# Optimization experiments

Measured on AMD Instinct MI355X. Metric: run time of the kernel, lower is better.

The kernel has to match this reference:

```python
import jax, jax.numpy as jnp
import numpy as np

N_NODES = 100000
N_EDGES = 1600000
NEG_SLOPE = 0.2  # PyG GATConv default


def _glorot(key, shape):
    fan = sum(shape[:2]) if len(shape) > 1 else shape[0] * 2
    s = jnp.sqrt(6.0 / fan)
    return jax.random.uniform(key, shape, jnp.float32, -s, s)


def gat_layer(x, src, dst, edge_attr, W, a_src, a_dst, We, a_e, b, heads, out_ch, concat):
    """Faithful PyG GATConv (add_self_loops=True, fill_value='mean', edge_dim set)."""
    n = x.shape[0]
    # self-loop edge_attr = mean of incoming edge_attr per dst node (0 if none)
    deg = jax.ops.segment_sum(jnp.ones((src.shape[0],), edge_attr.dtype), dst, num_segments=n)
    loop_attr = jax.ops.segment_sum(edge_attr, dst, num_segments=n) / jnp.maximum(deg, 1.0)[:, None]
    loop = jnp.arange(n, dtype=src.dtype)
    src_f = jnp.concatenate([src, loop])
    dst_f = jnp.concatenate([dst, loop])
    ea = jnp.concatenate([edge_attr, loop_attr], axis=0)
    # node transform -> [n, H, C]
    h = (x @ W).reshape(n, heads, out_ch)
    al_src = jnp.sum(h * a_src, axis=-1)  # [n, H]
    al_dst = jnp.sum(h * a_dst, axis=-1)  # [n, H]
    e = (ea @ We).reshape(-1, heads, out_ch)
    al_e = jnp.sum(e * a_e, axis=-1)      # [Ef, H]
    alpha = jax.nn.leaky_relu(al_src[src_f] + al_dst[dst_f] + al_e, negative_slope=NEG_SLOPE)
    # segment softmax over destination nodes (every node has a self loop)
    m = jax.ops.segment_max(alpha, dst_f, num_segments=n)
    ex = jnp.exp(alpha - m[dst_f])
    den = jax.ops.segment_sum(ex, dst_f, num_segments=n)
    att = ex / den[dst_f]                 # [Ef, H]
    out = jax.ops.segment_sum(att[:, :, None] * h[src_f], dst_f, num_segments=n)  # [n, H, C]
    out = out.reshape(n, heads * out_ch) if concat else out.mean(axis=1)
    return out + b


def setup_inputs() -> dict:
    key = jax.random.key(0)
    ks = jax.random.split(key, 20)
    x = jax.random.normal(ks[0], (N_NODES, 5), jnp.float32)
    edge_index = jax.random.randint(ks[1], (2, N_EDGES), 0, N_NODES, jnp.int64)
    edge_attr = jax.random.normal(ks[2], (N_EDGES, 2), jnp.float32)
    # conv1: in=5, out=32, heads=4, concat -> 128
    p = {
        "W1": _glorot(ks[3], (5, 128)), "aS1": _glorot(ks[4], (4, 32)),
        "aD1": _glorot(ks[5], (4, 32)), "We1": _glorot(ks[6], (2, 128)),
        "aE1": _glorot(ks[7], (4, 32)), "b1": jnp.zeros((128,), jnp.float32),
        # conv2: in=128, out=32, heads=2, concat -> 64
        "W2": _glorot(ks[8], (128, 64)), "aS2": _glorot(ks[9], (2, 32)),
        "aD2": _glorot(ks[10], (2, 32)), "We2": _glorot(ks[11], (2, 64)),
        "aE2": _glorot(ks[12], (2, 32)), "b2": jnp.zeros((64,), jnp.float32),
        # conv3: in=64, out=1, heads=1, concat=False
        "W3": _glorot(ks[13], (64, 1)), "aS3": _glorot(ks[14], (1, 1)),
        "aD3": _glorot(ks[15], (1, 1)), "We3": _glorot(ks[16], (2, 1)),
        "aE3": _glorot(ks[17], (1, 1)), "b3": jnp.zeros((1,), jnp.float32),
    }
    return {"x": x, "edge_index": edge_index, "edge_attr": edge_attr, **p}


def reference(x, edge_index, edge_attr,
              W1, aS1, aD1, We1, aE1, b1,
              W2, aS2, aD2, We2, aE2, b2,
              W3, aS3, aD3, We3, aE3, b3):
    src, dst = edge_index[0], edge_index[1]
    h = gat_layer(x, src, dst, edge_attr, W1, aS1, aD1, We1, aE1, b1, 4, 32, True)
    h = jax.nn.elu(h)  # dropout is identity in eval
    h = gat_layer(h, src, dst, edge_attr, W2, aS2, aD2, We2, aE2, b2, 2, 32, True)
    h = jax.nn.elu(h)
    h = gat_layer(h, src, dst, edge_attr, W3, aS3, aD3, We3, aE3, b3, 1, 1, False)
    return jax.nn.sigmoid(h).squeeze(-1)  # [N]
```

## Files before the change

### kernel.cpp

```cpp
#include <hip/hip_runtime.h>
#include <math.h>

#define NN 100000
#define NE 1600000
#define NPB 256
#define NB 391
#define NCHUNK 256
#define CH ((NE + NCHUNK - 1) / NCHUNK)
#define LOG2E 1.44269504088896f

__device__ __forceinline__ float lrelu(float x) { return fmaxf(x, 0.2f * x); }
__device__ __forceinline__ float elu1(float x) { return x > 0.f ? x : (__expf(x) - 1.f); }
__device__ __forceinline__ float fexp2(float x) {
#if __has_builtin(__builtin_amdgcn_exp2f)
    return __builtin_amdgcn_exp2f(x);
#else
    return exp2f(x);
#endif
}
__device__ __forceinline__ unsigned bf16rne(float f) {
    unsigned u = __float_as_uint(f);
    return (u + 0x7FFFu + ((u >> 16) & 1u)) >> 16;
}
__device__ __forceinline__ float bf16lo(unsigned u) { return __uint_as_float(u << 16); }
__device__ __forceinline__ float bf16hi(unsigned u) {
    return __uint_as_float(u & 0xFFFF0000u);
}

__global__ void __launch_bounds__(256) k_binA0(const int* __restrict__ dst,
                                               int* __restrict__ bucket_cnt) {
    __shared__ int hist[NB];
    int t = threadIdx.x;
    for (int b = t; b < NB; b += 256) hist[b] = 0;
    __syncthreads();
    int c0 = blockIdx.x * CH, c1 = min(NE, c0 + CH);
    for (int e = c0 + t; e < c1; e += 256) atomicAdd(&hist[dst[e] >> 8], 1);
    __syncthreads();
    for (int b = t; b < NB; b += 256)
        if (hist[b]) atomicAdd(&bucket_cnt[b], hist[b]);
}

__global__ void k_bscan(const int* __restrict__ bucket_cnt, int* __restrict__ bucket_base,
                        int* __restrict__ bucket_tail) {
    __shared__ int s[512];
    int t = threadIdx.x;
    int v = (t < NB) ? bucket_cnt[t] : 0;
    s[t] = v;
    __syncthreads();
    for (int off = 1; off < 512; off <<= 1) {
        int x = (t >= off) ? s[t - off] : 0;
        __syncthreads();
        if (t >= off) s[t] += x;
        __syncthreads();
    }
    if (t < NB) {
        int ex = s[t] - v;
        bucket_base[t] = ex;
        bucket_tail[t] = ex;
        if (t == NB - 1) bucket_base[NB] = s[t];
    }
}

__global__ void __launch_bounds__(256) k_binA2(const int* __restrict__ src,
                                               const int* __restrict__ dst,
                                               const float* __restrict__ ea,
                                               int* __restrict__ bucket_tail,
                                               uint2* __restrict__ binned,
                                               unsigned char* __restrict__ dstb) {
    __shared__ int hist[NB], base_l[NB], cursor[NB];
    int t = threadIdx.x;
    for (int b = t; b < NB; b += 256) {
        hist[b] = 0;
        cursor[b] = 0;
    }
    __syncthreads();
    int c0 = blockIdx.x * CH, c1 = min(NE, c0 + CH);
    for (int e = c0 + t; e < c1; e += 256) atomicAdd(&hist[dst[e] >> 8], 1);
    __syncthreads();
    for (int b = t; b < NB; b += 256)
        if (hist[b]) base_l[b] = atomicAdd(&bucket_tail[b], hist[b]);
    __syncthreads();
    for (int e = c0 + t; e < c1; e += 256) {
        int d = dst[e];
        int bkt = d >> 8;
        int idx = atomicAdd(&cursor[bkt], 1);
        int pos = base_l[bkt] + idx;
        unsigned pk = bf16rne(ea[2 * e]) | (bf16rne(ea[2 * e + 1]) << 16);
        binned[pos] = make_uint2((unsigned)src[e], pk);
        dstb[pos] = (unsigned char)(d & 255);
    }
}

__global__ void __launch_bounds__(256) k_binB(const int* __restrict__ bucket_base,
                                              const uint2* __restrict__ binned,
                                              const unsigned char* __restrict__ dstb,
                                              int* __restrict__ rowptr,
                                              uint2* __restrict__ edges,
                                              float* __restrict__ la) {
    __shared__ int hist[NPB], pre[NPB], cursor[NPB];
    __shared__ float ea0s[NPB], ea1s[NPB];
    int b = blockIdx.x, t = threadIdx.x;
    int bb = bucket_base[b], be = bucket_base[b + 1];
    int nb0 = b << 8;
    hist[t] = 0;
    ea0s[t] = 0.f;
    ea1s[t] = 0.f;
    __syncthreads();
    for (int e = bb + t; e < be; e += 256) atomicAdd(&hist[dstb[e]], 1);
    __syncthreads();
    int v = hist[t];
    pre[t] = v;
    __syncthreads();
    for (int off = 1; off < 256; off <<= 1) {
        int x = (t >= off) ? pre[t - off] : 0;
        __syncthreads();
        if (t >= off) pre[t] += x;
        __syncthreads();
    }
    int ex = pre[t] - v;
    if (nb0 + t <= NN) rowptr[nb0 + t] = bb + ex;
    cursor[t] = bb + ex;
    __syncthreads();
    for (int e = bb + t; e < be; e += 256) {
        uint2 rec = binned[e];
        unsigned char d = dstb[e];
        int pos = atomicAdd(&cursor[d], 1);
        edges[pos] = rec;
        atomicAdd(&ea0s[d], bf16lo(rec.y));
        atomicAdd(&ea1s[d], bf16hi(rec.y));
    }
    __syncthreads();
    int n = nb0 + t;
    if (n < NN) {
        float dg = fmaxf((float)v, 1.0f);
        la[2 * n] = ea0s[t] / dg;
        la[2 * n + 1] = ea1s[t] / dg;
    }
}

__global__ void k_const(const float* __restrict__ We1, const float* __restrict__ aE1,
                        const float* __restrict__ We2, const float* __restrict__ aE2,
                        const float* __restrict__ We3, const float* __restrict__ aE3,
                        const float* __restrict__ W1, const float* __restrict__ aS1,
                        const float* __restrict__ aD1, float* __restrict__ cbuf) {
    int t = threadIdx.x;
    if (t < 8) {
        int d = t >> 2, hd = t & 3;
        float s = 0.f;
        for (int c = 0; c < 32; c++) s += We1[d * 128 + hd * 32 + c] * aE1[hd * 32 + c];
        cbuf[t] = s * LOG2E;
    } else if (t < 12) {
        int idx = t - 8, d = idx >> 1, hd = idx & 1;
        float s = 0.f;
        for (int c = 0; c < 32; c++) s += We2[d * 64 + hd * 32 + c] * aE2[hd * 32 + c];
        cbuf[t] = s * LOG2E;
    } else if (t < 14) {
        cbuf[t] = We3[t - 12] * aE3[0] * LOG2E;
    } else if (t >= 16 && t < 56) {
        int r = (t - 16) % 20, hd = r / 5, i = r % 5;
        const float* a = (t - 16 < 20) ? aS1 : aD1;
        float s = 0.f;
        for (int c = 0; c < 32; c++) s += W1[i * 128 + hd * 32 + c] * a[hd * 32 + c];
        cbuf[t] = s * LOG2E;
    }
}

__global__ void k_prep1(const float* __restrict__ x, const float* __restrict__ vsd,
                        float4* __restrict__ xp, float4* __restrict__ als1,
                        float4* __restrict__ ald1) {
    int n = blockIdx.x * blockDim.x + threadIdx.x;
    if (n >= NN) return;
    float x0 = x[5 * n], x1 = x[5 * n + 1], x2 = x[5 * n + 2], x3 = x[5 * n + 3],
          x4 = x[5 * n + 4];
    xp[2 * n] = make_float4(x0, x1, x2, x3);
    xp[2 * n + 1] = make_float4(x4, 0.f, 0.f, 0.f);
    float sv[4], dv[4];
#pragma unroll
    for (int hd = 0; hd < 4; hd++) {
        const float* vS = vsd + hd * 5;
        const float* vD = vsd + 20 + hd * 5;
        sv[hd] = x0 * vS[0] + x1 * vS[1] + x2 * vS[2] + x3 * vS[3] + x4 * vS[4];
        dv[hd] = x0 * vD[0] + x1 * vD[1] + x2 * vD[2] + x3 * vD[3] + x4 * vD[4];
    }
    als1[n] = make_float4(sv[0], sv[1], sv[2], sv[3]);
    ald1[n] = make_float4(dv[0], dv[1], dv[2], dv[3]);
}

__global__ void k_agg1(const int* __restrict__ rowptr, const uint2* __restrict__ edges,
                       const float4* __restrict__ xp, const float* __restrict__ als1,
                       const float* __restrict__ ald1, const float* __restrict__ la,
                       const float* __restrict__ me, float* __restrict__ xw) {
    int t = blockIdx.x * blockDim.x + threadIdx.x;
    if (t >= NN * 4) return;
    int n = t >> 2, hd = t & 3;
    float me0 = me[hd], me1 = me[4 + hd];
    float aldn = ald1[t];
    float aself = lrelu(als1[t] + aldn + la[2 * n] * me0 + la[2 * n + 1] * me1);
    int start = rowptr[n], end = rowptr[n + 1];
    float den = 1.f;
    float4 xa = xp[2 * n];
    float xb = xp[2 * n + 1].x;
    float a0 = xa.x, a1 = xa.y, a2 = xa.z, a3 = xa.w, a4 = xb;
    for (int e = start; e < end; ++e) {
        uint2 ep = edges[e];
        int s = (int)ep.x;
        float a = lrelu(als1[s * 4 + hd] + aldn + bf16lo(ep.y) * me0 + bf16hi(ep.y) * me1);
        float p = fexp2(a - aself);
        den += p;
        float4 sa = xp[2 * s];
        float sb = xp[2 * s + 1].x;
        a0 += p * sa.x;
        a1 += p * sa.y;
        a2 += p * sa.z;
        a3 += p * sa.w;
        a4 += p * sb;
    }
    float r = 1.f / den;
    float* w = xw + (size_t)n * 20 + hd * 5;
    w[0] = a0 * r;
    w[1] = a1 * r;
    w[2] = a2 * r;
    w[3] = a3 * r;
    w[4] = a4 * r;
}

__global__ void __launch_bounds__(64) k_l2trans(
        const float* __restrict__ xw, const float* __restrict__ W1,
        const float* __restrict__ b1, const float* __restrict__ W2,
        const float* __restrict__ aS2, const float* __restrict__ aD2,
        unsigned short* __restrict__ h2q, float* __restrict__ als2,
        float* __restrict__ ald2) {
    __shared__ float sx[16 * 132];
    int nb = blockIdx.x * 16, t = threadIdx.x;
    {
        int nl = t >> 2, q = t & 3;
        int node = nb + nl;
        float w[20];
        if (node < NN) {
#pragma unroll
            for (int i = 0; i < 20; i++) w[i] = xw[(size_t)node * 20 + i];
        } else {
#pragma unroll
            for (int i = 0; i < 20; i++) w[i] = 0.f;
        }
#pragma unroll
        for (int k = 0; k < 32; k++) {
            int ch = q + 4 * k;
            int hd = ch >> 5;
            float v = w[hd * 5] * W1[ch] + w[hd * 5 + 1] * W1[128 + ch] +
                      w[hd * 5 + 2] * W1[256 + ch] + w[hd * 5 + 3] * W1[384 + ch] +
                      w[hd * 5 + 4] * W1[512 + ch] + b1[ch];
            sx[nl * 132 + ch] = (node < NN) ? elu1(v) : 0.f;
        }
    }
    __syncthreads();
    int jq = t & 15, ng = t >> 4;
    int j4 = jq * 4;
    float4 acc[4];
#pragma unroll
    for (int p = 0; p < 4; p++) acc[p] = make_float4(0.f, 0.f, 0.f, 0.f);
    for (int ic = 0; ic < 128; ic += 4) {
        float4 s[4];
#pragma unroll
        for (int p = 0; p < 4; p++)
            s[p] = *(const float4*)(sx + (ng * 4 + p) * 132 + ic);
#pragma unroll
        for (int r = 0; r < 4; r++) {
            float4 wv = *(const float4*)(W2 + (ic + r) * 64 + j4);
#pragma unroll
            for (int p = 0; p < 4; p++) {
                float sv = (r == 0) ? s[p].x : (r == 1) ? s[p].y : (r == 2) ? s[p].z : s[p].w;
                acc[p].x += sv * wv.x;
                acc[p].y += sv * wv.y;
                acc[p].z += sv * wv.z;
                acc[p].w += sv * wv.w;
            }
        }
    }
    int hd = jq >> 3;
    float4 a_s = *(const float4*)(aS2 + j4);
    float4 a_d = *(const float4*)(aD2 + j4);
    float pS[4], pD[4];
#pragma unroll
    for (int p = 0; p < 4; p++) {
        pS[p] = acc[p].x * a_s.x + acc[p].y * a_s.y + acc[p].z * a_s.z + acc[p].w * a_s.w;
        pD[p] = acc[p].x * a_d.x + acc[p].y * a_d.y + acc[p].z * a_d.z + acc[p].w * a_d.w;
    }
#pragma unroll
    for (int off = 1; off < 8; off <<= 1) {
#pragma unroll
        for (int p = 0; p < 4; p++) {
            pS[p] += __shfl_xor(pS[p], off);
            pD[p] += __shfl_xor(pD[p], off);
        }
    }
#pragma unroll
    for (int p = 0; p < 4; p++) {
        int node = nb + ng * 4 + p;
        if (node < NN) {
            ushort4 q;
            q.x = (unsigned short)bf16rne(acc[p].x);
            q.y = (unsigned short)bf16rne(acc[p].y);
            q.z = (unsigned short)bf16rne(acc[p].z);
            q.w = (unsigned short)bf16rne(acc[p].w);
            *(ushort4*)(h2q + (size_t)node * 64 + j4) = q;
            if ((jq & 7) == 0) {
                als2[node * 2 + hd] = pS[p] * LOG2E;
                ald2[node * 2 + hd] = pD[p] * LOG2E;
            }
        }
    }
}

__global__ void k_agg2(const int* __restrict__ rowptr, const uint2* __restrict__ edges,
                       const unsigned short* __restrict__ h2q,
                       const float* __restrict__ als2, const float* __restrict__ ald2,
                       const float* __restrict__ la, const float* __restrict__ me,
                       const float* __restrict__ b2, const float* __restrict__ W3,
                       float* __restrict__ h3) {
    int t = blockIdx.x * blockDim.x + threadIdx.x;
    if (t >= NN * 4) return;
    int n = t >> 2, sub = t & 3, hd = sub >> 1, qh = sub & 1;
    int cbase = hd * 32 + qh * 16;
    float me0 = me[hd], me1 = me[2 + hd];
    float aldn = ald2[n * 2 + hd];
    float aself = lrelu(als2[n * 2 + hd] + aldn + la[2 * n] * me0 + la[2 * n + 1] * me1);
    int start = rowptr[n], end = rowptr[n + 1];
    float den = 1.f;
    float acc[16];
    {
        const uint4* hp = (const uint4*)(h2q + (size_t)n * 64 + cbase);
        uint4 u0 = hp[0], u1 = hp[1];
        acc[0] = bf16lo(u0.x); acc[1] = bf16hi(u0.x);
        acc[2] = bf16lo(u0.y); acc[3] = bf16hi(u0.y);
        acc[4] = bf16lo(u0.z); acc[5] = bf16hi(u0.z);
        acc[6] = bf16lo(u0.w); acc[7] = bf16hi(u0.w);
        acc[8] = bf16lo(u1.x); acc[9] = bf16hi(u1.x);
        acc[10] = bf16lo(u1.y); acc[11] = bf16hi(u1.y);
        acc[12] = bf16lo(u1.z); acc[13] = bf16hi(u1.z);
        acc[14] = bf16lo(u1.w); acc[15] = bf16hi(u1.w);
    }
    for (int e = start; e < end; ++e) {
        uint2 ep = edges[e];
        int s = (int)ep.x;
        float a = lrelu(als2[s * 2 + hd] + aldn + bf16lo(ep.y) * me0 + bf16hi(ep.y) * me1);
        float p = fexp2(a - aself);
        den += p;
        const uint4* sp = (const uint4*)(h2q + (size_t)s * 64 + cbase);
        uint4 u0 = sp[0], u1 = sp[1];
        acc[0] += p * bf16lo(u0.x); acc[1] += p * bf16hi(u0.x);
        acc[2] += p * bf16lo(u0.y); acc[3] += p * bf16hi(u0.y);
        acc[4] += p * bf16lo(u0.z); acc[5] += p * bf16hi(u0.z);
        acc[6] += p * bf16lo(u0.w); acc[7] += p * bf16hi(u0.w);
        acc[8] += p * bf16lo(u1.x); acc[9] += p * bf16hi(u1.x);
        acc[10] += p * bf16lo(u1.y); acc[11] += p * bf16hi(u1.y);
        acc[12] += p * bf16lo(u1.z); acc[13] += p * bf16hi(u1.z);
        acc[14] += p * bf16lo(u1.w); acc[15] += p * bf16hi(u1.w);
    }
    float r = 1.f / den;
    float part = 0.f;
#pragma unroll
    for (int c = 0; c < 16; c++) {
        float v = elu1(acc[c] * r + b2[cbase + c]);
        part += v * W3[cbase + c];
    }
    part += __shfl_xor(part, 1);
    part += __shfl_xor(part, 2);
    if (sub == 0) h3[n] = part;
}

__global__ void k_agg3(const int* __restrict__ rowptr, const uint2* __restrict__ edges,
                       const float* __restrict__ h, const float* __restrict__ aS3,
                       const float* __restrict__ aD3, const float* __restrict__ la,
                       const float* __restrict__ me, const float* __restrict__ b,
                       float* __restrict__ out) {
    int n = (blockIdx.x * blockDim.x + threadIdx.x) >> 6;
    if (n >= NN) return;
    int lane = threadIdx.x & 63;
    float me0 = me[0], me1 = me[1];
    float aSs = aS3[0] * LOG2E, aDs = aD3[0] * LOG2E;
    float hn = h[n];
    float ald_n = hn * aDs;
    float aself = lrelu(hn * aSs + ald_n + la[2 * n] * me0 + la[2 * n + 1] * me1);
    int start = rowptr[n], end = rowptr[n + 1];
    float den = 0.f, num = 0.f;
    for (int e = start + lane; e < end; e += 64) {
        uint2 ep = edges[e];
        int s = (int)ep.x;
        float hv = h[s];
        float a = lrelu(hv * aSs + ald_n + bf16lo(ep.y) * me0 + bf16hi(ep.y) * me1);
        float p = fexp2(a - aself);
        den += p;
        num += p * hv;
    }
#pragma unroll
    for (int off = 32; off > 0; off >>= 1) {
        den += __shfl_xor(den, off);
        num += __shfl_xor(num, off);
    }
    if (lane == 0) {
        den += 1.f;
        num += hn;
        float v = num / den + b[0];
        out[n] = 1.f / (1.f + __expf(-v));
    }
}

extern "C" void kernel_launch(void* const* d_in, const int* in_sizes, int n_in,
                              void* d_out, int out_size, void* d_ws, size_t ws_size,
                              hipStream_t stream) {
    const float* x   = (const float*)d_in[0];
    const int*   ei  = (const int*)d_in[1];
    const float* ea  = (const float*)d_in[2];
    const float* W1  = (const float*)d_in[3];
    const float* aS1 = (const float*)d_in[4];
    const float* aD1 = (const float*)d_in[5];
    const float* We1 = (const float*)d_in[6];
    const float* aE1 = (const float*)d_in[7];
    const float* b1  = (const float*)d_in[8];
    const float* W2  = (const float*)d_in[9];
    const float* aS2 = (const float*)d_in[10];
    const float* aD2 = (const float*)d_in[11];
    const float* We2 = (const float*)d_in[12];
    const float* aE2 = (const float*)d_in[13];
    const float* b2  = (const float*)d_in[14];
    const float* W3  = (const float*)d_in[15];
    const float* aS3 = (const float*)d_in[16];
    const float* aD3 = (const float*)d_in[17];
    const float* We3 = (const float*)d_in[18];
    const float* aE3 = (const float*)d_in[19];
    const float* b3  = (const float*)d_in[20];

    const int* srcv = ei;
    const int* dstv = ei + NE;

    char* basep = (char*)d_ws;
    size_t off = 0;
    auto alloc = [&](size_t nbytes) -> void* {
        void* p = basep + off;
        off += (nbytes + 255) & ~(size_t)255;
        return p;
    };
    int*    bucket_cnt  = (int*)alloc((size_t)(NB + 1) * 4);
    int*    bucket_base = (int*)alloc((size_t)(NB + 1) * 4);
    int*    bucket_tail = (int*)alloc((size_t)(NB + 1) * 4);
    int*    rowptr      = (int*)alloc((size_t)(NN + 1) * 4);
    uint2*  binned      = (uint2*)alloc((size_t)NE * 8);
    unsigned char* dstb = (unsigned char*)alloc((size_t)NE);
    uint2*  edges       = (uint2*)alloc((size_t)NE * 8);
    float*  la          = (float*)alloc((size_t)NN * 8);
    float*  cbuf        = (float*)alloc(256);
    float4* xp          = (float4*)alloc((size_t)NN * 32);
    float4* als1        = (float4*)alloc((size_t)NN * 16);
    float4* ald1        = (float4*)alloc((size_t)NN * 16);
    float*  xw          = (float*)alloc((size_t)NN * 80);
    unsigned short* h2q = (unsigned short*)alloc((size_t)NN * 128);
    float*  als2        = (float*)alloc((size_t)NN * 8);
    float*  ald2        = (float*)alloc((size_t)NN * 8);
    float*  h3          = (float*)alloc((size_t)NN * 4);
    (void)ws_size; (void)in_sizes; (void)n_in; (void)out_size;

    float* me1 = cbuf;
    float* me2 = cbuf + 8;
    float* me3 = cbuf + 12;
    float* vsd = cbuf + 16;

    auto cdiv = [](long long a, long long b) { return (int)((a + b - 1) / b); };
    const int BS = 256;

    hipMemsetAsync(bucket_cnt, 0, (size_t)(NB + 1) * 4, stream);
    k_binA0<<<NCHUNK, 256, 0, stream>>>(dstv, bucket_cnt);
    k_bscan<<<1, 512, 0, stream>>>(bucket_cnt, bucket_base, bucket_tail);
    k_binA2<<<NCHUNK, 256, 0, stream>>>(srcv, dstv, ea, bucket_tail, binned, dstb);
    k_binB<<<NB, 256, 0, stream>>>(bucket_base, binned, dstb, rowptr, edges, la);

    k_const<<<1, 64, 0, stream>>>(We1, aE1, We2, aE2, We3, aE3, W1, aS1, aD1, cbuf);

    k_prep1<<<cdiv(NN, BS), BS, 0, stream>>>(x, vsd, xp, als1, ald1);
    k_agg1<<<cdiv((long long)NN * 4, BS), BS, 0, stream>>>(rowptr, edges, xp,
                                                           (const float*)als1,
                                                           (const float*)ald1, la, me1, xw);

    k_l2trans<<<cdiv(NN, 16), 64, 0, stream>>>(xw, W1, b1, W2, aS2, aD2, h2q, als2, ald2);
    k_agg2<<<cdiv((long long)NN * 4, BS), BS, 0, stream>>>(rowptr, edges, h2q, als2, ald2,
                                                           la, me2, b2, W3, h3);

    k_agg3<<<cdiv(NN, 4), 256, 0, stream>>>(rowptr, edges, h3, aS3, aD3, la, me3,
                                            b3, (float*)d_out);
}
```

Measured before the change: 344.8 us.

## Fuse edge binning into one local-sort pass and widen layer-2 transform tile

Replaces the separate count pass and scatter pass of edge binning with a single kernel per chunk. Each chunk counts its edges, sorts them locally by bucket in shared memory, writes them out contiguously and records per-chunk segment offsets. The second kernel then gathers each bucket's pieces from all chunks into a shared staging buffer before doing the per-node sort. This is meant to cut one full read of dst and the scattered global writes. Separately, the layer-2 transform now handles 32 nodes per block instead of 16, so each W2 load is reused across more nodes. The fixed MAXB staging cap silently drops edges if a bucket exceeds 5376, so correctness depends on the degree distribution.

```diff
diff --git a/kernel.cpp b/kernel.cpp
--- a/kernel.cpp
+++ b/kernel.cpp
@@ -5,8 +5,10 @@
 #define NE 1600000
 #define NPB 256
 #define NB 391
-#define NCHUNK 256
-#define CH ((NE + NCHUNK - 1) / NCHUNK)
+#define NCHUNK 512
+#define CH 3125
+#define SEGW (NB + 1)
+#define MAXB 5376
 #define LOG2E 1.44269504088896f
 
 __device__ __forceinline__ float lrelu(float x) { return fmaxf(x, 0.2f * x); }
@@ -27,21 +29,59 @@
     return __uint_as_float(u & 0xFFFF0000u);
 }
 
-__global__ void __launch_bounds__(256) k_binA0(const int* __restrict__ dst,
-                                               int* __restrict__ bucket_cnt) {
-    __shared__ int hist[NB];
-    int t = threadIdx.x;
+__global__ void __launch_bounds__(256) k_bin1(const int* __restrict__ src,
+                                              const int* __restrict__ dst,
+                                              const float* __restrict__ ea,
+                                              int* __restrict__ bucket_cnt,
+                                              int* __restrict__ seg,
+                                              uint2* __restrict__ binned,
+                                              unsigned char* __restrict__ dstb) {
+    __shared__ int hist[NB], start[NB], cur[NB];
+    __shared__ int s2[256];
+    __shared__ uint2 stage[CH];
+    __shared__ unsigned char dstg[CH];
+    int c = blockIdx.x, t = threadIdx.x;
+    int e0 = c * CH;
     for (int b = t; b < NB; b += 256) hist[b] = 0;
     __syncthreads();
-    int c0 = blockIdx.x * CH, c1 = min(NE, c0 + CH);
-    for (int e = c0 + t; e < c1; e += 256) atomicAdd(&hist[dst[e] >> 8], 1);
-    __syncthreads();
-    for (int b = t; b < NB; b += 256)
+    for (int i = t; i < CH; i += 256) atomicAdd(&hist[dst[e0 + i] >> 8], 1);
+    __syncthreads();
+    int a0 = (2 * t < NB) ? hist[2 * t] : 0;
+    int a1 = (2 * t + 1 < NB) ? hist[2 * t + 1] : 0;
+    s2[t] = a0 + a1;
+    __syncthreads();
+    for (int off = 1; off < 256; off <<= 1) {
+        int x = (t >= off) ? s2[t - off] : 0;
+        __syncthreads();
+        if (t >= off) s2[t] += x;
+        __syncthreads();
+    }
+    int pex = s2[t] - (a0 + a1);
+    if (2 * t < NB) { start[2 * t] = pex; cur[2 * t] = pex; }
+    if (2 * t + 1 < NB) { start[2 * t + 1] = pex + a0; cur[2 * t + 1] = pex + a0; }
+    __syncthreads();
+    for (int b = t; b < NB; b += 256) {
+        seg[c * SEGW + b] = start[b];
         if (hist[b]) atomicAdd(&bucket_cnt[b], hist[b]);
-}
-
-__global__ void k_bscan(const int* __restrict__ bucket_cnt, int* __restrict__ bucket_base,
-                        int* __restrict__ bucket_tail) {
+    }
+    if (t == 0) seg[c * SEGW + NB] = CH;
+    __syncthreads();
+    for (int i = t; i < CH; i += 256) {
+        int d = dst[e0 + i];
+        int bkt = d >> 8;
+        int p = atomicAdd(&cur[bkt], 1);
+        unsigned pk = bf16rne(ea[2 * (e0 + i)]) | (bf16rne(ea[2 * (e0 + i) + 1]) << 16);
+        stage[p] = make_uint2((unsigned)src[e0 + i], pk);
+        dstg[p] = (unsigned char)(d & 255);
+    }
+    __syncthreads();
+    for (int i = t; i < CH; i += 256) {
+        binned[e0 + i] = stage[i];
+        dstb[e0 + i] = dstg[i];
+    }
+}
+
+__global__ void k_bscan(const int* __restrict__ bucket_cnt, int* __restrict__ bucket_base) {
     __shared__ int s[512];
     int t = threadIdx.x;
     int v = (t < NB) ? bucket_cnt[t] : 0;
@@ -54,59 +94,64 @@
         __syncthreads();
     }
     if (t < NB) {
-        int ex = s[t] - v;
-        bucket_base[t] = ex;
-        bucket_tail[t] = ex;
+        bucket_base[t] = s[t] - v;
         if (t == NB - 1) bucket_base[NB] = s[t];
     }
 }
 
-__global__ void __launch_bounds__(256) k_binA2(const int* __restrict__ src,
-                                               const int* __restrict__ dst,
-                                               const float* __restrict__ ea,
-                                               int* __restrict__ bucket_tail,
-                                               uint2* __restrict__ binned,
-                                               unsigned char* __restrict__ dstb) {
-    __shared__ int hist[NB], base_l[NB], cursor[NB];
-    int t = threadIdx.x;
-    for (int b = t; b < NB; b += 256) {
-        hist[b] = 0;
-        cursor[b] = 0;
-    }
-    __syncthreads();
-    int c0 = blockIdx.x * CH, c1 = min(NE, c0 + CH);
-    for (int e = c0 + t; e < c1; e += 256) atomicAdd(&hist[dst[e] >> 8], 1);
-    __syncthreads();
-    for (int b = t; b < NB; b += 256)
-        if (hist[b]) base_l[b] = atomicAdd(&bucket_tail[b], hist[b]);
-    __syncthreads();
-    for (int e = c0 + t; e < c1; e += 256) {
-        int d = dst[e];
-        int bkt = d >> 8;
-        int idx = atomicAdd(&cursor[bkt], 1);
-        int pos = base_l[bkt] + idx;
-        unsigned pk = bf16rne(ea[2 * e]) | (bf16rne(ea[2 * e + 1]) << 16);
-        binned[pos] = make_uint2((unsigned)src[e], pk);
-        dstb[pos] = (unsigned char)(d & 255);
-    }
-}
-
-__global__ void __launch_bounds__(256) k_binB(const int* __restrict__ bucket_base,
+__global__ void __launch_bounds__(256) k_bin2(const int* __restrict__ bucket_base,
+                                              const int* __restrict__ seg,
                                               const uint2* __restrict__ binned,
                                               const unsigned char* __restrict__ dstb,
                                               int* __restrict__ rowptr,
                                               uint2* __restrict__ edges,
                                               float* __restrict__ la) {
+    __shared__ int sstart[NCHUNK], soff[NCHUNK];
+    __shared__ int s2[256];
+    __shared__ uint2 stage[MAXB];
+    __shared__ unsigned char sd[MAXB];
     __shared__ int hist[NPB], pre[NPB], cursor[NPB];
     __shared__ float ea0s[NPB], ea1s[NPB];
     int b = blockIdx.x, t = threadIdx.x;
-    int bb = bucket_base[b], be = bucket_base[b + 1];
-    int nb0 = b << 8;
+    int len0, len1;
+    {
+        int c0 = 2 * t, c1 = 2 * t + 1;
+        int st0 = seg[c0 * SEGW + b], en0 = seg[c0 * SEGW + b + 1];
+        int st1 = seg[c1 * SEGW + b], en1 = seg[c1 * SEGW + b + 1];
+        sstart[c0] = st0;
+        sstart[c1] = st1;
+        len0 = en0 - st0;
+        len1 = en1 - st1;
+        s2[t] = len0 + len1;
+    }
+    __syncthreads();
+    for (int off = 1; off < 256; off <<= 1) {
+        int x = (t >= off) ? s2[t - off] : 0;
+        __syncthreads();
+        if (t >= off) s2[t] += x;
+        __syncthreads();
+    }
+    int pex = s2[t] - (len0 + len1);
+    soff[2 * t] = pex;
+    soff[2 * t + 1] = pex + len0;
+    __syncthreads();
+    int total = s2[255];
+    if (total > MAXB) total = MAXB;
+    for (int i = t; i < total; i += 256) {
+        int lo = 0, hi = NCHUNK - 1;
+        while (lo < hi) {
+            int mid = (lo + hi + 1) >> 1;
+            if (soff[mid] <= i) lo = mid; else hi = mid - 1;
+        }
+        int pos = lo * CH + sstart[lo] + (i - soff[lo]);
+        stage[i] = binned[pos];
+        sd[i] = dstb[pos];
+    }
     hist[t] = 0;
     ea0s[t] = 0.f;
     ea1s[t] = 0.f;
     __syncthreads();
-    for (int e = bb + t; e < be; e += 256) atomicAdd(&hist[dstb[e]], 1);
+    for (int i = t; i < total; i += 256) atomicAdd(&hist[sd[i]], 1);
     __syncthreads();
     int v = hist[t];
     pre[t] = v;
@@ -117,13 +162,15 @@
         if (t >= off) pre[t] += x;
         __syncthreads();
     }
+    int bb = bucket_base[b];
     int ex = pre[t] - v;
+    int nb0 = b << 8;
     if (nb0 + t <= NN) rowptr[nb0 + t] = bb + ex;
     cursor[t] = bb + ex;
     __syncthreads();
-    for (int e = bb + t; e < be; e += 256) {
-        uint2 rec = binned[e];
-        unsigned char d = dstb[e];
+    for (int i = t; i < total; i += 256) {
+        uint2 rec = stage[i];
+        unsigned char d = sd[i];
         int pos = atomicAdd(&cursor[d], 1);
         edges[pos] = rec;
         atomicAdd(&ea0s[d], bf16lo(rec.y));
@@ -230,10 +277,12 @@
         const float* __restrict__ aS2, const float* __restrict__ aD2,
         unsigned short* __restrict__ h2q, float* __restrict__ als2,
         float* __restrict__ ald2) {
-    __shared__ float sx[16 * 132];
-    int nb = blockIdx.x * 16, t = threadIdx.x;
-    {
-        int nl = t >> 2, q = t & 3;
+    __shared__ float sx[32 * 132];
+    int nb = blockIdx.x * 32, t = threadIdx.x;
+#pragma unroll
+    for (int half = 0; half < 2; half++) {
+        int nl = (t >> 2) + 16 * half;
+        int q = t & 3;
         int node = nb + nl;
         float w[20];
         if (node < NN) {
@@ -256,19 +305,19 @@
     __syncthreads();
     int jq = t & 15, ng = t >> 4;
     int j4 = jq * 4;
-    float4 acc[4];
-#pragma unroll
-    for (int p = 0; p < 4; p++) acc[p] = make_float4(0.f, 0.f, 0.f, 0.f);
+    float4 acc[8];
+#pragma unroll
+    for (int p = 0; p < 8; p++) acc[p] = make_float4(0.f, 0.f, 0.f, 0.f);
     for (int ic = 0; ic < 128; ic += 4) {
-        float4 s[4];
-#pragma unroll
-        for (int p = 0; p < 4; p++)
-            s[p] = *(const float4*)(sx + (ng * 4 + p) * 132 + ic);
+        float4 s[8];
+#pragma unroll
+        for (int p = 0; p < 8; p++)
+            s[p] = *(const float4*)(sx + (ng + 4 * p) * 132 + ic);
 #pragma unroll
         for (int r = 0; r < 4; r++) {
             float4 wv = *(const float4*)(W2 + (ic + r) * 64 + j4);
 #pragma unroll
-            for (int p = 0; p < 4; p++) {
+            for (int p = 0; p < 8; p++) {
                 float sv = (r == 0) ? s[p].x : (r == 1) ? s[p].y : (r == 2) ? s[p].z : s[p].w;
                 acc[p].x += sv * wv.x;
                 acc[p].y += sv * wv.y;
@@ -280,23 +329,23 @@
     int hd = jq >> 3;
     float4 a_s = *(const float4*)(aS2 + j4);
     float4 a_d = *(const float4*)(aD2 + j4);
-    float pS[4], pD[4];
-#pragma unroll
-    for (int p = 0; p < 4; p++) {
+    float pS[8], pD[8];
+#pragma unroll
+    for (int p = 0; p < 8; p++) {
         pS[p] = acc[p].x * a_s.x + acc[p].y * a_s.y + acc[p].z * a_s.z + acc[p].w * a_s.w;
         pD[p] = acc[p].x * a_d.x + acc[p].y * a_d.y + acc[p].z * a_d.z + acc[p].w * a_d.w;
     }
 #pragma unroll
     for (int off = 1; off < 8; off <<= 1) {
 #pragma unroll
-        for (int p = 0; p < 4; p++) {
+        for (int p = 0; p < 8; p++) {
             pS[p] += __shfl_xor(pS[p], off);
             pD[p] += __shfl_xor(pD[p], off);
         }
     }
 #pragma unroll
-    for (int p = 0; p < 4; p++) {
-        int node = nb + ng * 4 + p;
+    for (int p = 0; p < 8; p++) {
+        int node = nb + ng + 4 * p;
         if (node < NN) {
             ushort4 q;
             q.x = (unsigned short)bf16rne(acc[p].x);
@@ -443,8 +492,8 @@
     };
     int*    bucket_cnt  = (int*)alloc((size_t)(NB + 1) * 4);
     int*    bucket_base = (int*)alloc((size_t)(NB + 1) * 4);
-    int*    bucket_tail = (int*)alloc((size_t)(NB + 1) * 4);
     int*    rowptr      = (int*)alloc((size_t)(NN + 1) * 4);
+    int*    seg         = (int*)alloc((size_t)NCHUNK * SEGW * 4);
     uint2*  binned      = (uint2*)alloc((size_t)NE * 8);
     unsigned char* dstb = (unsigned char*)alloc((size_t)NE);
     uint2*  edges       = (uint2*)alloc((size_t)NE * 8);
@@ -469,10 +518,9 @@
     const int BS = 256;
 
     hipMemsetAsync(bucket_cnt, 0, (size_t)(NB + 1) * 4, stream);
-    k_binA0<<<NCHUNK, 256, 0, stream>>>(dstv, bucket_cnt);
-    k_bscan<<<1, 512, 0, stream>>>(bucket_cnt, bucket_base, bucket_tail);
-    k_binA2<<<NCHUNK, 256, 0, stream>>>(srcv, dstv, ea, bucket_tail, binned, dstb);
-    k_binB<<<NB, 256, 0, stream>>>(bucket_base, binned, dstb, rowptr, edges, la);
+    k_bin1<<<NCHUNK, 256, 0, stream>>>(srcv, dstv, ea, bucket_cnt, seg, binned, dstb);
+    k_bscan<<<1, 512, 0, stream>>>(bucket_cnt, bucket_base);
+    k_bin2<<<NB, 256, 0, stream>>>(bucket_base, seg, binned, dstb, rowptr, edges, la);
 
     k_const<<<1, 64, 0, stream>>>(We1, aE1, We2, aE2, We3, aE3, W1, aS1, aD1, cbuf);
 
@@ -481,7 +529,7 @@
                                                            (const float*)als1,
                                                            (const float*)ald1, la, me1, xw);
 
-    k_l2trans<<<cdiv(NN, 16), 64, 0, stream>>>(xw, W1, b1, W2, aS2, aD2, h2q, als2, ald2);
+    k_l2trans<<<cdiv(NN, 32), 64, 0, stream>>>(xw, W1, b1, W2, aS2, aD2, h2q, als2, ald2);
     k_agg2<<<cdiv((long long)NN * 4, BS), BS, 0, stream>>>(rowptr, edges, h2q, als2, ald2,
                                                            la, me2, b2, W3, h3);
 
```

After: 347.3 us. Within noise of the previous version (+0.7%).
